# Optimization experiments

Hardware: AMD Instinct MI355X
Metric: run time of the kernel (lower is better)

The kernel has to match this reference:

```python
import jax, jax.numpy as jnp
import numpy as np

WIDTH = 1024

def setup_inputs() -> dict:
    key = jax.random.key(0)
    ks = jax.random.split(key, 5)
    x = jax.random.normal(ks[0], (4, 4096, WIDTH), dtype=jnp.float32)
    # LayerNorm params
    ln_gamma = jnp.ones((WIDTH,), dtype=jnp.float32)
    ln_beta = jnp.zeros((WIDTH,), dtype=jnp.float32)
    # Linear params (torch nn.Linear init: U(-1/sqrt(fan_in), 1/sqrt(fan_in)))
    bound = 1.0 / np.sqrt(WIDTH)
    w1 = jax.random.uniform(ks[1], (WIDTH, WIDTH), jnp.float32, -bound, bound)
    b1 = jax.random.uniform(ks[2], (WIDTH,), jnp.float32, -bound, bound)
    w2 = jax.random.uniform(ks[3], (WIDTH, WIDTH), jnp.float32, -bound, bound)
    b2 = jax.random.uniform(ks[4], (WIDTH,), jnp.float32, -bound, bound)
    return {"x": x, "ln_gamma": ln_gamma, "ln_beta": ln_beta,
            "w1": w1, "b1": b1, "w2": w2, "b2": b2}

def _layernorm(x, gamma, beta, eps=1e-5):
    mu = jnp.mean(x, axis=-1, keepdims=True)
    var = jnp.mean(jnp.square(x - mu), axis=-1, keepdims=True)
    return (x - mu) * jax.lax.rsqrt(var + eps) * gamma + beta

def reference(x, ln_gamma, ln_beta, w1, b1, w2, b2):
    # Pre-norm residual MLP: x + W2 @ gelu(W1 @ LN(x) + b1) + b2
    h = _layernorm(x, ln_gamma, ln_beta)
    h = jnp.einsum('bsd,ed->bse', h, w1) + b1  # w stored as [out, in] like torch
    h = jax.nn.gelu(h, approximate=False)      # torch nn.GELU default = exact erf
    # dropout p=0.0 -> identity
    h = jnp.einsum('bsd,ed->bse', h, w2) + b2
    return x + h
```

## Files before the change

kernel.cpp:

```cpp
#include <hip/hip_runtime.h>
#include <hip/hip_bf16.h>
#include <math.h>

typedef __bf16 bf16x8 __attribute__((ext_vector_type(8)));
typedef float f32x4 __attribute__((ext_vector_type(4)));

#define GAS __attribute__((address_space(1)))
#define LAS __attribute__((address_space(3)))

static __device__ __forceinline__ void load16(const void* g, void* l) {
    __builtin_amdgcn_global_load_lds((const GAS void*)g, (LAS void*)l, 16, 0, 0);
}

struct __align__(8) bh4 { __hip_bfloat16 x, y, z, w; };

__global__ __launch_bounds__(256) void pre_kernel(
        const float* __restrict__ x, const float* __restrict__ gamma,
        const float* __restrict__ beta, const float* __restrict__ w1,
        const float* __restrict__ w2, __hip_bfloat16* __restrict__ hn,
        __hip_bfloat16* __restrict__ w1b, __hip_bfloat16* __restrict__ w2b, int nln) {
    if ((int)blockIdx.x >= nln) {
        const int i = (blockIdx.x - nln) * 256 + threadIdx.x;
        float4 a = ((const float4*)w1)[i];
        float4 b = ((const float4*)w2)[i];
        bh4 r1, r2;
        r1.x = __float2bfloat16(a.x); r1.y = __float2bfloat16(a.y);
        r1.z = __float2bfloat16(a.z); r1.w = __float2bfloat16(a.w);
        r2.x = __float2bfloat16(b.x); r2.y = __float2bfloat16(b.y);
        r2.z = __float2bfloat16(b.z); r2.w = __float2bfloat16(b.w);
        ((bh4*)w1b)[i] = r1;
        ((bh4*)w2b)[i] = r2;
        return;
    }
    const int row  = (blockIdx.x << 2) + (threadIdx.x >> 6);
    const int lane = threadIdx.x & 63;
    const float4* px = (const float4*)(x + (size_t)row * 1024);
    float4 v[4];
    float s = 0.f;
#pragma unroll
    for (int i = 0; i < 4; ++i) {
        v[i] = px[lane + (i << 6)];
        s += v[i].x + v[i].y + v[i].z + v[i].w;
    }
#pragma unroll
    for (int o = 32; o; o >>= 1) s += __shfl_xor(s, o, 64);
    const float mu = s * (1.0f / 1024.0f);
    float vs = 0.f;
#pragma unroll
    for (int i = 0; i < 4; ++i) {
        float a = v[i].x - mu, b = v[i].y - mu, c = v[i].z - mu, d = v[i].w - mu;
        vs += a * a + b * b + c * c + d * d;
    }
#pragma unroll
    for (int o = 32; o; o >>= 1) vs += __shfl_xor(vs, o, 64);
    const float rs = rsqrtf(vs * (1.0f / 1024.0f) + 1e-5f);
    const float4* pg = (const float4*)gamma;
    const float4* pb = (const float4*)beta;
    bh4* po = (bh4*)(hn + (size_t)row * 1024);
#pragma unroll
    for (int i = 0; i < 4; ++i) {
        const int idx = lane + (i << 6);
        float4 g = pg[idx], bb = pb[idx];
        bh4 r;
        r.x = __float2bfloat16((v[i].x - mu) * rs * g.x + bb.x);
        r.y = __float2bfloat16((v[i].y - mu) * rs * g.y + bb.y);
        r.z = __float2bfloat16((v[i].z - mu) * rs * g.z + bb.z);
        r.w = __float2bfloat16((v[i].w - mu) * rs * g.w + bb.w);
        po[idx] = r;
    }
}

__device__ __forceinline__ float gelu_exact(float v) {
    const float ax = fabsf(v) * 0.70710678118654752f;
    const float t  = __builtin_amdgcn_rcpf(__builtin_fmaf(0.3275911f, ax, 1.0f));
    float p = __builtin_fmaf(1.061405429f, t, -1.453152027f);
    p = __builtin_fmaf(p, t, 1.421413741f);
    p = __builtin_fmaf(p, t, -0.284496736f);
    p = __builtin_fmaf(p, t, 0.254829592f);
    p *= t;
    const float e  = __expf(-ax * ax);
    const float er = __builtin_fmaf(-p, e, 1.0f);
    return 0.5f * v * (1.0f + copysignf(er, v));
}

#define SCB() __builtin_amdgcn_sched_barrier(0)
#define BAR() do { __builtin_amdgcn_s_barrier(); SCB(); } while (0)
#define LGKM0() do { asm volatile("s_waitcnt lgkmcnt(0)" ::: "memory"); SCB(); } while (0)
#define VMW(n) do { asm volatile("s_waitcnt vmcnt(" #n ")" ::: "memory"); SCB(); } while (0)

__device__ __forceinline__ void rdA(const char* base, bf16x8 (&aF)[4][2], int px0, int px1) {
#pragma unroll
    for (int ii = 0; ii < 4; ++ii) {
        aF[ii][0] = *(const bf16x8*)(base + ii * 2048 + px0);
        aF[ii][1] = *(const bf16x8*)(base + ii * 2048 + px1);
    }
}
__device__ __forceinline__ void rdB(const char* base, bf16x8 (&bF)[2][2], int px0, int px1) {
#pragma unroll
    for (int jj = 0; jj < 2; ++jj) {
        bF[jj][0] = *(const bf16x8*)(base + jj * 128 + px0);
        bF[jj][1] = *(const bf16x8*)(base + jj * 128 + px1);
    }
}
template <int MI, int NI>
__device__ __forceinline__ void mfmaQ(f32x4 (&acc)[8][4], const bf16x8 (&aF)[4][2],
                                      const bf16x8 (&bF)[2][2]) {
    __builtin_amdgcn_s_setprio(1);
#pragma unroll
    for (int ii = 0; ii < 4; ++ii)
#pragma unroll
        for (int jj = 0; jj < 2; ++jj) {
            acc[MI * 4 + ii][NI * 2 + jj] = __builtin_amdgcn_mfma_f32_16x16x32_bf16(
                aF[ii][0], bF[jj][0], acc[MI * 4 + ii][NI * 2 + jj], 0, 0, 0);
            acc[MI * 4 + ii][NI * 2 + jj] = __builtin_amdgcn_mfma_f32_16x16x32_bf16(
                aF[ii][1], bF[jj][1], acc[MI * 4 + ii][NI * 2 + jj], 0, 0, 0);
        }
    __builtin_amdgcn_s_setprio(0);
}

#define TILE(CUR, OTH, KOFF, SA_EN, SB_EN) do { \
    const char* aB_ = aRd + (CUR) * 32768; \
    const char* bB_ = bRd + (CUR) * 32768; \
    rdA(aB_, aF, px0, px1); \
    rdB(bB_, bF0, px0, px1); \
    if (SA_EN) { load16(aS0 + (KOFF) + 64, dA + (OTH) * 32768); \
                 load16(aS1 + (KOFF) + 64, dA + (OTH) * 32768 + 8192); } \
    BAR();                                   \
    LGKM0(); \
    mfmaQ<0, 0>(acc, aF, bF0); \
    rdB(bB_ + 256, bF1, px0, px1); \
    if (SA_EN) { load16(aS0 + 131072 + (KOFF) + 64, dA + (OTH) * 32768 + 16384); \
                 load16(aS1 + 131072 + (KOFF) + 64, dA + (OTH) * 32768 + 24576); } \
    LGKM0(); \
    mfmaQ<0, 1>(acc, aF, bF1); \
    BAR();                                   \
    rdA(aB_ + 8192, aF, px0, px1); \
    if (SB_EN) { load16(bS0 + (KOFF) + 128, dB + (CUR) * 32768); \
                 load16(bS1 + (KOFF) + 128, dB + (CUR) * 32768 + 8192); } \
    LGKM0(); \
    mfmaQ<1, 1>(acc, aF, bF1); \
    if (SB_EN) { load16(bS0 + 131072 + (KOFF) + 128, dB + (CUR) * 32768 + 16384); \
                 load16(bS1 + 131072 + (KOFF) + 128, dB + (CUR) * 32768 + 24576); } \
    mfmaQ<1, 0>(acc, aF, bF0); \
} while (0)

template <int EPI>
__global__ __launch_bounds__(512, 2) void gemm256(
        const __hip_bfloat16* __restrict__ A,
        const __hip_bfloat16* __restrict__ B,
        const float* __restrict__ bias,
        const float* __restrict__ resid,
        __hip_bfloat16* __restrict__ outb,
        float* __restrict__ outf) {
    constexpr int K = 1024, N = 1024;
    __shared__ __align__(16) char lds[131072];
    char* sA = lds;
    char* sB = lds + 65536;

    const int tid  = threadIdx.x;
    const int lane = tid & 63;
    const int w    = tid >> 6;
    const int wr   = w >> 2;
    const int wc   = w & 3;
    const int f    = lane & 15;
    const int h    = lane >> 4;
    const int bm   = blockIdx.x * 256;
    const int bn   = blockIdx.y * 256;

    const int cid0 = tid, cid1 = tid + 512;
    const __hip_bfloat16* aS0 = A + (size_t)(bm + (cid0 >> 3)) * K + (((cid0 & 7) ^ ((cid0 >> 3) & 7)) << 3);
    const __hip_bfloat16* aS1 = A + (size_t)(bm + (cid1 >> 3)) * K + (((cid1 & 7) ^ ((cid1 >> 3) & 7)) << 3);
    const __hip_bfloat16* bS0 = B + (size_t)(bn + (cid0 >> 3)) * K + (((cid0 & 7) ^ ((cid0 >> 5) & 7)) << 3);
    const __hip_bfloat16* bS1 = B + (size_t)(bn + (cid1 >> 3)) * K + (((cid1 & 7) ^ ((cid1 >> 5) & 7)) << 3);
    char* dA = sA + tid * 16;
    char* dB = sB + tid * 16;

    const int pxk = (f & 7) * 16;
    const int px0 = (h * 16) ^ pxk;
    const int px1 = ((4 + h) * 16) ^ pxk;
    const char* aRd = sA + (size_t)(wr * 128 + f) * 128;
    const char* bRd = sB + (size_t)(wc * 64 + 4 * f) * 128;

    f32x4 acc[8][4] = {};
    bf16x8 aF[4][2], bF0[2][2], bF1[2][2];

    load16(bS0, dB);                  load16(bS1, dB + 8192);
    load16(bS0 + 131072, dB + 16384); load16(bS1 + 131072, dB + 24576);
    load16(aS0, dA);                  load16(aS1, dA + 8192);
    load16(aS0 + 131072, dA + 16384); load16(aS1 + 131072, dA + 24576);
    load16(bS0 + 64, dB + 32768);             load16(bS1 + 64, dB + 32768 + 8192);
    load16(bS0 + 131072 + 64, dB + 32768 + 16384); load16(bS1 + 131072 + 64, dB + 32768 + 24576);
    VMW(4);
    BAR();

#pragma unroll 1
    for (int it = 0; it < 7; ++it) {
        const int k0 = it << 7;
        TILE(0, 1, k0, true, true);
        VMW(4); BAR();
        TILE(1, 0, k0 + 64, true, true);
        VMW(4); BAR();
    }
    TILE(0, 1, 896, true, false);
    VMW(0); BAR();
    TILE(1, 0, 960, false, false);

    const int colb = bn + wc * 64 + f * 4;
    const float4 bias4 = *(const float4*)(bias + colb);
#pragma unroll
    for (int i = 0; i < 8; ++i) {
#pragma unroll
        for (int r = 0; r < 4; ++r) {
            const size_t grow = (size_t)(bm + wr * 128 + i * 16 + h * 4 + r);
            float v0 = acc[i][0][r] + bias4.x;
            float v1 = acc[i][1][r] + bias4.y;
            float v2 = acc[i][2][r] + bias4.z;
            float v3 = acc[i][3][r] + bias4.w;
            if (EPI == 0) {
                bh4 o;
                o.x = __float2bfloat16(gelu_exact(v0));
                o.y = __float2bfloat16(gelu_exact(v1));
                o.z = __float2bfloat16(gelu_exact(v2));
                o.w = __float2bfloat16(gelu_exact(v3));
                *(bh4*)(outb + grow * N + colb) = o;
            } else {
                const float4 rs = *(const float4*)(resid + grow * N + colb);
                float4 o = {v0 + rs.x, v1 + rs.y, v2 + rs.z, v3 + rs.w};
                *(float4*)(outf + grow * N + colb) = o;
            }
        }
    }
}

extern "C" void kernel_launch(void* const* d_in, const int* in_sizes, int n_in,
                              void* d_out, int out_size, void* d_ws, size_t ws_size,
                              hipStream_t stream) {
    const float* x     = (const float*)d_in[0];
    const float* gamma = (const float*)d_in[1];
    const float* beta  = (const float*)d_in[2];
    const float* w1    = (const float*)d_in[3];
    const float* b1    = (const float*)d_in[4];
    const float* w2    = (const float*)d_in[5];
    const float* b2    = (const float*)d_in[6];
    float* out = (float*)d_out;

    const int M = in_sizes[0] / 1024;

    char* ws = (char*)d_ws;
    __hip_bfloat16* hn  = (__hip_bfloat16*)ws;
    __hip_bfloat16* h1  = (__hip_bfloat16*)(ws + (size_t)M * 2048);
    __hip_bfloat16* w1b = (__hip_bfloat16*)(ws + (size_t)M * 4096);
    __hip_bfloat16* w2b = (__hip_bfloat16*)(ws + (size_t)M * 4096 + 2097152);

    const int nln = M / 4;
    pre_kernel<<<nln + 1024, 256, 0, stream>>>(x, gamma, beta, w1, w2, hn, w1b, w2b, nln);
    gemm256<0><<<dim3(M / 256, 4), 512, 0, stream>>>(hn, w1b, b1, nullptr, h1, nullptr);
    gemm256<1><<<dim3(M / 256, 4), 512, 0, stream>>>(h1, w2b, b2, x, nullptr, out);
}
```

Before: 211.1 us.

## Reschedule GEMM global-to-LDS prefetch across quarter-tile barriers

Reorders which halves of the A and B tiles are prefetched into LDS during each quarter of the k-tile. The prologue now preloads the first halves of both A and B for the next stage instead of all of B. Each MFMA quarter is wrapped in barriers, with a partial lgkmcnt wait added before the first one. The aim is to spread the direct-to-LDS loads more evenly against the MFMA work. The extra barriers add synchronization cost, and the new ordering of buffer writes against reads may create hazards.

```diff
diff --git a/kernel.cpp b/kernel.cpp
--- a/kernel.cpp
+++ b/kernel.cpp
@@ -86,6 +86,7 @@
 #define SCB() __builtin_amdgcn_sched_barrier(0)
 #define BAR() do { __builtin_amdgcn_s_barrier(); SCB(); } while (0)
 #define LGKM0() do { asm volatile("s_waitcnt lgkmcnt(0)" ::: "memory"); SCB(); } while (0)
+#define LGKMH() do { asm volatile("s_waitcnt lgkmcnt(8)" ::: "memory"); SCB(); } while (0)
 #define VMW(n) do { asm volatile("s_waitcnt vmcnt(" #n ")" ::: "memory"); SCB(); } while (0)
 
 __device__ __forceinline__ void rdA(const char* base, bf16x8 (&aF)[4][2], int px0, int px1) {
@@ -118,30 +119,30 @@
     __builtin_amdgcn_s_setprio(0);
 }
 
-#define TILE(CUR, OTH, KOFF, SA_EN, SB_EN) do { \
+#define TILE(CUR, OTH, KOFF, S1, S2) do { \
     const char* aB_ = aRd + (CUR) * 32768; \
     const char* bB_ = bRd + (CUR) * 32768; \
+     \
     rdA(aB_, aF, px0, px1); \
     rdB(bB_, bF0, px0, px1); \
-    if (SA_EN) { load16(aS0 + (KOFF) + 64, dA + (OTH) * 32768); \
-                 load16(aS1 + (KOFF) + 64, dA + (OTH) * 32768 + 8192); } \
-    BAR();                                   \
-    LGKM0(); \
-    mfmaQ<0, 0>(acc, aF, bF0); \
+    if (S1) { load16(aS0 + 131072 + (KOFF) + 64, dA + (OTH) * 32768 + 16384); \
+              load16(aS1 + 131072 + (KOFF) + 64, dA + (OTH) * 32768 + 24576); } \
+    LGKMH(); \
+    BAR(); LGKM0(); mfmaQ<0, 0>(acc, aF, bF0); BAR(); \
+     \
     rdB(bB_ + 256, bF1, px0, px1); \
-    if (SA_EN) { load16(aS0 + 131072 + (KOFF) + 64, dA + (OTH) * 32768 + 16384); \
-                 load16(aS1 + 131072 + (KOFF) + 64, dA + (OTH) * 32768 + 24576); } \
-    LGKM0(); \
-    mfmaQ<0, 1>(acc, aF, bF1); \
-    BAR();                                   \
+    if (S1) { load16(bS0 + 131072 + (KOFF) + 64, dB + (OTH) * 32768 + 16384); \
+              load16(bS1 + 131072 + (KOFF) + 64, dB + (OTH) * 32768 + 24576); } \
+    BAR(); LGKM0(); mfmaQ<0, 1>(acc, aF, bF1); BAR(); \
+     \
     rdA(aB_ + 8192, aF, px0, px1); \
-    if (SB_EN) { load16(bS0 + (KOFF) + 128, dB + (CUR) * 32768); \
-                 load16(bS1 + (KOFF) + 128, dB + (CUR) * 32768 + 8192); } \
-    LGKM0(); \
-    mfmaQ<1, 1>(acc, aF, bF1); \
-    if (SB_EN) { load16(bS0 + 131072 + (KOFF) + 128, dB + (CUR) * 32768 + 16384); \
-                 load16(bS1 + 131072 + (KOFF) + 128, dB + (CUR) * 32768 + 24576); } \
-    mfmaQ<1, 0>(acc, aF, bF0); \
+    if (S2) { load16(bS0 + (KOFF) + 128, dB + (CUR) * 32768); \
+              load16(bS1 + (KOFF) + 128, dB + (CUR) * 32768 + 8192); } \
+    BAR(); LGKM0(); mfmaQ<1, 1>(acc, aF, bF1); BAR(); \
+     \
+    if (S2) { load16(aS0 + (KOFF) + 128, dA + (CUR) * 32768); \
+              load16(aS1 + (KOFF) + 128, dA + (CUR) * 32768 + 8192); } \
+    BAR(); mfmaQ<1, 0>(acc, aF, bF0); \
 } while (0)
 
 template <int EPI>
@@ -188,8 +189,8 @@
     load16(bS0 + 131072, dB + 16384); load16(bS1 + 131072, dB + 24576);
     load16(aS0, dA);                  load16(aS1, dA + 8192);
     load16(aS0 + 131072, dA + 16384); load16(aS1 + 131072, dA + 24576);
-    load16(bS0 + 64, dB + 32768);             load16(bS1 + 64, dB + 32768 + 8192);
-    load16(bS0 + 131072 + 64, dB + 32768 + 16384); load16(bS1 + 131072 + 64, dB + 32768 + 24576);
+    load16(bS0 + 64, dB + 32768);     load16(bS1 + 64, dB + 32768 + 8192);
+    load16(aS0 + 64, dA + 32768);     load16(aS1 + 64, dA + 32768 + 8192);
     VMW(4);
     BAR();
 
```

Measured after the change: 212.1 us. No clear change (+0.5%).

## Restructure GEMM K-loop pipeline to single barrier per tile with partial LDS waits

Applied to the files above, without the earlier changes.

Reorganizes the per-tile schedule of the bf16 GEMM: all LDS fragment reads are issued up front, the intra-tile barriers are removed, and a partial lgkmcnt wait lets the first MFMA group start before every read has landed. The B-operand prefetch now goes to the other buffer together with A, instead of running one stage further ahead into the current buffer. The goal is to cut barrier stalls and overlap LDS reads with MFMA work. In exchange, each tile now waits for all outstanding global loads (vmcnt 0) before its barrier, which removes the earlier deeper B prefetch and can expose global load latency.

```diff
diff --git a/kernel.cpp b/kernel.cpp
--- a/kernel.cpp
+++ b/kernel.cpp
@@ -85,7 +85,7 @@
 
 #define SCB() __builtin_amdgcn_sched_barrier(0)
 #define BAR() do { __builtin_amdgcn_s_barrier(); SCB(); } while (0)
-#define LGKM0() do { asm volatile("s_waitcnt lgkmcnt(0)" ::: "memory"); SCB(); } while (0)
+#define LGKM(n) do { asm volatile("s_waitcnt lgkmcnt(" #n ")" ::: "memory"); SCB(); } while (0)
 #define VMW(n) do { asm volatile("s_waitcnt vmcnt(" #n ")" ::: "memory"); SCB(); } while (0)
 
 __device__ __forceinline__ void rdA(const char* base, bf16x8 (&aF)[4][2], int px0, int px1) {
@@ -118,29 +118,27 @@
     __builtin_amdgcn_s_setprio(0);
 }
 
-#define TILE(CUR, OTH, KOFF, SA_EN, SB_EN) do { \
+#define TILE(CUR, OTH, KOFF, S1) do { \
     const char* aB_ = aRd + (CUR) * 32768; \
     const char* bB_ = bRd + (CUR) * 32768; \
-    rdA(aB_, aF, px0, px1); \
-    rdB(bB_, bF0, px0, px1); \
-    if (SA_EN) { load16(aS0 + (KOFF) + 64, dA + (OTH) * 32768); \
-                 load16(aS1 + (KOFF) + 64, dA + (OTH) * 32768 + 8192); } \
-    BAR();                                   \
-    LGKM0(); \
+    if (S1) { load16(aS0 + (KOFF) + 64, dA + (OTH) * 32768); \
+              load16(aS1 + (KOFF) + 64, dA + (OTH) * 32768 + 8192); } \
+    rdB(bB_, bF0, px0, px1); SCB(); \
+    rdA(aB_, aF, px0, px1); SCB(); \
+    rdB(bB_ + 256, bF1, px0, px1); SCB(); \
+    if (S1) { load16(aS0 + 131072 + (KOFF) + 64, dA + (OTH) * 32768 + 16384); \
+              load16(aS1 + 131072 + (KOFF) + 64, dA + (OTH) * 32768 + 24576); } \
+    LGKM(4); \
     mfmaQ<0, 0>(acc, aF, bF0); \
-    rdB(bB_ + 256, bF1, px0, px1); \
-    if (SA_EN) { load16(aS0 + 131072 + (KOFF) + 64, dA + (OTH) * 32768 + 16384); \
-                 load16(aS1 + 131072 + (KOFF) + 64, dA + (OTH) * 32768 + 24576); } \
-    LGKM0(); \
+    if (S1) { load16(bS0 + (KOFF) + 64, dB + (OTH) * 32768); \
+              load16(bS1 + (KOFF) + 64, dB + (OTH) * 32768 + 8192); } \
+    LGKM(0); \
     mfmaQ<0, 1>(acc, aF, bF1); \
-    BAR();                                   \
-    rdA(aB_ + 8192, aF, px0, px1); \
-    if (SB_EN) { load16(bS0 + (KOFF) + 128, dB + (CUR) * 32768); \
-                 load16(bS1 + (KOFF) + 128, dB + (CUR) * 32768 + 8192); } \
-    LGKM0(); \
+    rdA(aB_ + 8192, aF, px0, px1); SCB(); \
+    if (S1) { load16(bS0 + 131072 + (KOFF) + 64, dB + (OTH) * 32768 + 16384); \
+              load16(bS1 + 131072 + (KOFF) + 64, dB + (OTH) * 32768 + 24576); } \
+    LGKM(0); \
     mfmaQ<1, 1>(acc, aF, bF1); \
-    if (SB_EN) { load16(bS0 + 131072 + (KOFF) + 128, dB + (CUR) * 32768 + 16384); \
-                 load16(bS1 + 131072 + (KOFF) + 128, dB + (CUR) * 32768 + 24576); } \
     mfmaQ<1, 0>(acc, aF, bF0); \
 } while (0)
 
@@ -188,22 +186,20 @@
     load16(bS0 + 131072, dB + 16384); load16(bS1 + 131072, dB + 24576);
     load16(aS0, dA);                  load16(aS1, dA + 8192);
     load16(aS0 + 131072, dA + 16384); load16(aS1 + 131072, dA + 24576);
-    load16(bS0 + 64, dB + 32768);             load16(bS1 + 64, dB + 32768 + 8192);
-    load16(bS0 + 131072 + 64, dB + 32768 + 16384); load16(bS1 + 131072 + 64, dB + 32768 + 24576);
-    VMW(4);
+    VMW(0);
     BAR();
 
 #pragma unroll 1
     for (int it = 0; it < 7; ++it) {
         const int k0 = it << 7;
-        TILE(0, 1, k0, true, true);
-        VMW(4); BAR();
-        TILE(1, 0, k0 + 64, true, true);
-        VMW(4); BAR();
-    }
-    TILE(0, 1, 896, true, false);
+        TILE(0, 1, k0, true);
+        VMW(0); BAR();
+        TILE(1, 0, k0 + 64, true);
+        VMW(0); BAR();
+    }
+    TILE(0, 1, 896, true);
     VMW(0); BAR();
-    TILE(1, 0, 960, false, false);
+    TILE(1, 0, 960, false);
 
     const int colb = bn + wc * 64 + f * 4;
     const float4 bias4 = *(const float4*)(bias + colb);
```

After: 206.0 us. 2.4% less time.
